# Optimization experiments

Hardware: AMD Instinct MI355X
Metric: run time of the kernel (lower is better)

The kernel has to match this reference:

```python
import jax, jax.numpy as jnp
import numpy as np

B, N, T, F = 4, 256, 16, 128
H = 256

def setup_inputs() -> dict:
    key = jax.random.key(0)
    k1, k2, k3, k4, k5 = jax.random.split(key, 5)
    bound1 = 1.0 / np.sqrt(2 * F)
    bound2 = 1.0 / np.sqrt(H)
    return {
        "nodefeat": jax.random.normal(k1, (B, N, T, F), dtype=jnp.float32),
        "W1": jax.random.uniform(k2, (H, 2 * F), minval=-bound1, maxval=bound1, dtype=jnp.float32),
        "b1": jax.random.uniform(k3, (H,), minval=-bound1, maxval=bound1, dtype=jnp.float32),
        "W2": jax.random.uniform(k4, (1, H), minval=-bound2, maxval=bound2, dtype=jnp.float32),
        "b2": jax.random.uniform(k5, (1,), minval=-bound2, maxval=bound2, dtype=jnp.float32),
    }

def reference(nodefeat, W1, b1, W2, b2):
    # nodefeat: [B,N,T,F] -> mean over time -> h: [B,N,F]
    h = jnp.mean(nodefeat, axis=2)
    f = h.shape[-1]
    # Split W1 to avoid materializing the [B,N,N,2F] concat:
    # Linear(cat(h_i,h_j)) = h_i @ W1[:, :F].T + h_j @ W1[:, F:].T + b1
    a = jnp.einsum('bnf,hf->bnh', h, W1[:, :f])  # contribution of h_i
    c = jnp.einsum('bnf,hf->bnh', h, W1[:, f:])  # contribution of h_j
    pre = a[:, :, None, :] + c[:, None, :, :] + b1  # [B,N,N,H]
    act = jax.nn.relu(pre)
    logits = jnp.einsum('bijh,h->bij', act, W2[0]) + b2[0]  # [B,N,N]
    return logits
```

## Files before the change

kernel.cpp:

```cpp
#include <hip/hip_runtime.h>

#define B_ 4
#define N_ 256
#define T_ 16
#define F_ 128
#define H_ 256
#define BN_ (B_ * N_)

__global__ __launch_bounds__(1024) void lp_prep(const float* __restrict__ nf,
                                                const float* __restrict__ W1,
                                                float* __restrict__ hbar,
                                                float* __restrict__ W1T) {
    __shared__ float sT[64][65];
    const int tid = threadIdx.x;
    if (blockIdx.x < 128) {
        const int idx = blockIdx.x * 1024 + tid;
        const int bn  = idx >> 7;
        const int f   = idx & 127;
        const float* src = nf + (size_t)bn * (T_ * F_) + f;
        float s = 0.f;
#pragma unroll
        for (int t = 0; t < T_; ++t) s += src[t * F_];
        hbar[idx] = s * (1.0f / 16.0f);
    } else {
        const int t  = blockIdx.x - 128;
        const int y0 = (t >> 2) * 64;
        const int x0 = (t & 3) * 64;
        const int ty = tid >> 6;
        const int tx = tid & 63;
#pragma unroll
        for (int r = 0; r < 4; ++r)
            sT[r * 16 + ty][tx] = W1[(size_t)(y0 + r * 16 + ty) * 256 + (x0 + tx)];
        __syncthreads();
#pragma unroll
        for (int r = 0; r < 4; ++r)
            W1T[(size_t)(x0 + r * 16 + ty) * 256 + (y0 + tx)] = sT[tx][r * 16 + ty];
    }
}

__global__ __launch_bounds__(512) void lp_gemm(const float* __restrict__ hbar,
                                               const float* __restrict__ W1T,
                                               const float* __restrict__ b1,
                                               float* __restrict__ aT,
                                               float* __restrict__ cT) {
    __shared__ float red[16][4][128];

    const int tile8 = blockIdx.x >> 1;
    const int h0    = (blockIdx.x & 1) * 128;
    const int bn0   = tile8 * 8;
    const int b     = bn0 >> 8;
    const int tid   = threadIdx.x;
    const int kq    = __builtin_amdgcn_readfirstlane(tid >> 7);
    const int hl    = tid & 127;
    const int h     = h0 + hl;

    const float* wA = W1T + (size_t)(kq * 32) * H_ + h;
    const float* wC = W1T + (size_t)(F_ + kq * 32) * H_ + h;
    const float* hb = hbar + (size_t)bn0 * F_ + kq * 32;

    float acca[8] = {0.f, 0.f, 0.f, 0.f, 0.f, 0.f, 0.f, 0.f};
    float accc[8] = {0.f, 0.f, 0.f, 0.f, 0.f, 0.f, 0.f, 0.f};

#pragma unroll 4
    for (int kk = 0; kk < 32; ++kk) {
        const float wa = wA[(size_t)kk * H_];
        const float wc = wC[(size_t)kk * H_];
#pragma unroll
        for (int n = 0; n < 8; ++n) {
            const float hv = hb[n * F_ + kk];
            acca[n] = fmaf(hv, wa, acca[n]);
            accc[n] = fmaf(hv, wc, accc[n]);
        }
    }

#pragma unroll
    for (int n = 0; n < 8; ++n) {
        red[n][kq][hl]     = acca[n];
        red[8 + n][kq][hl] = accc[n];
    }
    __syncthreads();

    const int rv = tid >> 7;
#pragma unroll
    for (int i = 0; i < 4; ++i) {
        const int v = rv * 4 + i;
        const float s = (red[v][0][hl] + red[v][1][hl]) + (red[v][2][hl] + red[v][3][hl]);
        if (v < 8) {
            const int bn = bn0 + v;
            aT[((size_t)(bn >> 2) * H_ + h) * 4 + (bn & 3)] = s + b1[h];
        } else {
            const int n = v - 8;
            cT[((size_t)b * H_ + h) * N_ + ((bn0 & 255) + n)] = s;
        }
    }
}

__global__ __launch_bounds__(1024) void lp_k2(const float* __restrict__ aT,
                                              const float* __restrict__ cT,
                                              const float* __restrict__ W2,
                                              const float* __restrict__ b2,
                                              float* __restrict__ out) {
    __shared__ float pr[8][8][128];

    const int bx  = blockIdx.x;
    const int b   = bx >> 6;
    const int rr  = bx & 63;
    const int it  = rr >> 1;
    const int jh  = rr & 1;
    const int i0  = it * 8;
    const int j0  = jh * 128;
    const int bn0 = b * N_ + i0;

    const int tid = threadIdx.x;
    const int ho  = __builtin_amdgcn_readfirstlane(tid >> 7);
    const int jl  = tid & 127;

    const float* crow = cT + (size_t)b * (H_ * N_) + j0 + jl;
    const float* a0 = aT + (size_t)(bn0 >> 2) * (H_ * 4);
    const float* a1 = a0 + H_ * 4;
    const int h0 = ho * 32;

    float acc0 = 0.f, acc1 = 0.f, acc2 = 0.f, acc3 = 0.f;
    float acc4 = 0.f, acc5 = 0.f, acc6 = 0.f, acc7 = 0.f;

#pragma unroll 4
    for (int hh = 0; hh < 32; ++hh) {
        const int h = h0 + hh;
        const float  cj  = crow[(size_t)h * N_];
        const float  w   = W2[h];
        const float4 av0 = *(const float4*)(a0 + h * 4);
        const float4 av1 = *(const float4*)(a1 + h * 4);
        float x;
        x = av0.x + cj; acc0 = fmaf(fmaxf(x, 0.f), w, acc0);
        x = av0.y + cj; acc1 = fmaf(fmaxf(x, 0.f), w, acc1);
        x = av0.z + cj; acc2 = fmaf(fmaxf(x, 0.f), w, acc2);
        x = av0.w + cj; acc3 = fmaf(fmaxf(x, 0.f), w, acc3);
        x = av1.x + cj; acc4 = fmaf(fmaxf(x, 0.f), w, acc4);
        x = av1.y + cj; acc5 = fmaf(fmaxf(x, 0.f), w, acc5);
        x = av1.z + cj; acc6 = fmaf(fmaxf(x, 0.f), w, acc6);
        x = av1.w + cj; acc7 = fmaf(fmaxf(x, 0.f), w, acc7);
    }

    pr[ho][0][jl] = acc0;
    pr[ho][1][jl] = acc1;
    pr[ho][2][jl] = acc2;
    pr[ho][3][jl] = acc3;
    pr[ho][4][jl] = acc4;
    pr[ho][5][jl] = acc5;
    pr[ho][6][jl] = acc6;
    pr[ho][7][jl] = acc7;
    __syncthreads();

    const int oi = tid >> 7;
    const int oj = tid & 127;
    float s = 0.f;
#pragma unroll
    for (int o = 0; o < 8; ++o) s += pr[o][oi][oj];
    out[(size_t)(bn0 + oi) * N_ + j0 + oj] = s + b2[0];
}

extern "C" void kernel_launch(void* const* d_in, const int* in_sizes, int n_in,
                              void* d_out, int out_size, void* d_ws, size_t ws_size,
                              hipStream_t stream) {
    const float* nodefeat = (const float*)d_in[0];
    const float* W1       = (const float*)d_in[1];
    const float* b1       = (const float*)d_in[2];
    const float* W2       = (const float*)d_in[3];
    const float* b2       = (const float*)d_in[4];
    float* out = (float*)d_out;

    float* hbar = (float*)d_ws;
    float* W1T  = hbar + (size_t)BN_ * F_;
    float* aT   = W1T + 256 * 256;
    float* cT   = aT + (size_t)256 * H_ * 4;

    lp_prep<<<144, 1024, 0, stream>>>(nodefeat, W1, hbar, W1T);
    lp_gemm<<<256, 512, 0, stream>>>(hbar, W1T, b1, aT, cT);
    lp_k2<<<256, 1024, 0, stream>>>(aT, cT, W2, b2, out);
}
```

Measured before the change: 25.45 us.

## Fuse time-mean, W1 transpose and projection GEMM into one kernel

Merges the prep kernel (time-mean plus W1 transpose) and the projection GEMM into a single kernel. Each block computes the time-mean for its 8 nodes into shared memory, then stages W1 in transposed 64-column chunks through LDS and accumulates the a/c projections, so the hbar and W1T round trips to global memory and one launch go away. In exchange, every one of the 128 blocks reloads and transposes all of W1, grid size drops from 256 to 128 blocks, and the large LDS buffer may limit occupancy.

```diff
diff --git a/kernel.cpp b/kernel.cpp
--- a/kernel.cpp
+++ b/kernel.cpp
@@ -5,92 +5,95 @@
 #define T_ 16
 #define F_ 128
 #define H_ 256
-#define BN_ (B_ * N_)
 
-__global__ __launch_bounds__(1024) void lp_prep(const float* __restrict__ nf,
-                                                const float* __restrict__ W1,
-                                                float* __restrict__ hbar,
-                                                float* __restrict__ W1T) {
-    __shared__ float sT[64][65];
+__global__ __launch_bounds__(1024) void lp_ka(const float* __restrict__ nf,
+                                              const float* __restrict__ W1,
+                                              const float* __restrict__ b1,
+                                              float* __restrict__ aT,
+                                              float* __restrict__ cT) {
+    __shared__ float sh[8 * 128];
+    __shared__ float buf[64 * 257];
+
+    const int blk = blockIdx.x;
+    const int bn0 = blk * 8;
+    const int b   = bn0 >> 8;
+    const int n0  = bn0 & 255;
     const int tid = threadIdx.x;
-    if (blockIdx.x < 128) {
-        const int idx = blockIdx.x * 1024 + tid;
-        const int bn  = idx >> 7;
-        const int f   = idx & 127;
-        const float* src = nf + (size_t)bn * (T_ * F_) + f;
+
+    {
+        const int n = tid >> 7;
+        const int f = tid & 127;
+        const float* src = nf + (size_t)(bn0 + n) * (T_ * F_) + f;
         float s = 0.f;
 #pragma unroll
         for (int t = 0; t < T_; ++t) s += src[t * F_];
-        hbar[idx] = s * (1.0f / 16.0f);
-    } else {
-        const int t  = blockIdx.x - 128;
-        const int y0 = (t >> 2) * 64;
-        const int x0 = (t & 3) * 64;
-        const int ty = tid >> 6;
-        const int tx = tid & 63;
-#pragma unroll
-        for (int r = 0; r < 4; ++r)
-            sT[r * 16 + ty][tx] = W1[(size_t)(y0 + r * 16 + ty) * 256 + (x0 + tx)];
-        __syncthreads();
-#pragma unroll
-        for (int r = 0; r < 4; ++r)
-            W1T[(size_t)(x0 + r * 16 + ty) * 256 + (y0 + tx)] = sT[tx][r * 16 + ty];
+        sh[n * 128 + f] = s * (1.0f / 16.0f);
     }
-}
 
-__global__ __launch_bounds__(512) void lp_gemm(const float* __restrict__ hbar,
-                                               const float* __restrict__ W1T,
-                                               const float* __restrict__ b1,
-                                               float* __restrict__ aT,
-                                               float* __restrict__ cT) {
-    __shared__ float red[16][4][128];
-
-    const int tile8 = blockIdx.x >> 1;
-    const int h0    = (blockIdx.x & 1) * 128;
-    const int bn0   = tile8 * 8;
-    const int b     = bn0 >> 8;
-    const int tid   = threadIdx.x;
-    const int kq    = __builtin_amdgcn_readfirstlane(tid >> 7);
-    const int hl    = tid & 127;
-    const int h     = h0 + hl;
-
-    const float* wA = W1T + (size_t)(kq * 32) * H_ + h;
-    const float* wC = W1T + (size_t)(F_ + kq * 32) * H_ + h;
-    const float* hb = hbar + (size_t)bn0 * F_ + kq * 32;
+    const int kq = tid >> 8;
+    const int h  = tid & 255;
 
     float acca[8] = {0.f, 0.f, 0.f, 0.f, 0.f, 0.f, 0.f, 0.f};
     float accc[8] = {0.f, 0.f, 0.f, 0.f, 0.f, 0.f, 0.f, 0.f};
 
-#pragma unroll 4
-    for (int kk = 0; kk < 32; ++kk) {
-        const float wa = wA[(size_t)kk * H_];
-        const float wc = wC[(size_t)kk * H_];
 #pragma unroll
-        for (int n = 0; n < 8; ++n) {
-            const float hv = hb[n * F_ + kk];
-            acca[n] = fmaf(hv, wa, acca[n]);
-            accc[n] = fmaf(hv, wc, accc[n]);
+    for (int c = 0; c < 4; ++c) {
+        __syncthreads();
+#pragma unroll
+        for (int i = 0; i < 4; ++i) {
+            const int e  = i * 1024 + tid;
+            const int hh = e >> 4;
+            const int f4 = e & 15;
+            const float4 w = *(const float4*)(W1 + (size_t)hh * 256 + c * 64 + f4 * 4);
+            const int k0 = f4 * 4;
+            buf[(k0 + 0) * 257 + hh] = w.x;
+            buf[(k0 + 1) * 257 + hh] = w.y;
+            buf[(k0 + 2) * 257 + hh] = w.z;
+            buf[(k0 + 3) * 257 + hh] = w.w;
+        }
+        __syncthreads();
+        const int kb = (c & 1) * 64 + kq * 16;
+        if (c < 2) {
+#pragma unroll
+            for (int kk = 0; kk < 16; ++kk) {
+                const float w = buf[(kq * 16 + kk) * 257 + h];
+                const int kh = kb + kk;
+#pragma unroll
+                for (int n = 0; n < 8; ++n)
+                    acca[n] = fmaf(sh[n * 128 + kh], w, acca[n]);
+            }
+        } else {
+#pragma unroll
+            for (int kk = 0; kk < 16; ++kk) {
+                const float w = buf[(kq * 16 + kk) * 257 + h];
+                const int kh = kb + kk;
+#pragma unroll
+                for (int n = 0; n < 8; ++n)
+                    accc[n] = fmaf(sh[n * 128 + kh], w, accc[n]);
+            }
         }
     }
 
+    __syncthreads();
 #pragma unroll
     for (int n = 0; n < 8; ++n) {
-        red[n][kq][hl]     = acca[n];
-        red[8 + n][kq][hl] = accc[n];
+        buf[((n)     * 4 + kq) * 256 + h] = acca[n];
+        buf[((8 + n) * 4 + kq) * 256 + h] = accc[n];
     }
     __syncthreads();
 
-    const int rv = tid >> 7;
 #pragma unroll
     for (int i = 0; i < 4; ++i) {
-        const int v = rv * 4 + i;
-        const float s = (red[v][0][hl] + red[v][1][hl]) + (red[v][2][hl] + red[v][3][hl]);
+        const int o  = i * 1024 + tid;
+        const int v  = o >> 8;
+        const int hh = o & 255;
+        const float* p = buf + v * 4 * 256 + hh;
+        const float s = (p[0] + p[256]) + (p[512] + p[768]);
         if (v < 8) {
             const int bn = bn0 + v;
-            aT[((size_t)(bn >> 2) * H_ + h) * 4 + (bn & 3)] = s + b1[h];
+            aT[((size_t)(bn >> 2) * H_ + hh) * 4 + (bn & 3)] = s + b1[hh];
         } else {
-            const int n = v - 8;
-            cT[((size_t)b * H_ + h) * N_ + ((bn0 & 255) + n)] = s;
+            cT[((size_t)b * H_ + hh) * N_ + (n0 + (v - 8))] = s;
         }
     }
 }
@@ -169,12 +172,9 @@
     const float* b2       = (const float*)d_in[4];
     float* out = (float*)d_out;
 
-    float* hbar = (float*)d_ws;
-    float* W1T  = hbar + (size_t)BN_ * F_;
-    float* aT   = W1T + 256 * 256;
-    float* cT   = aT + (size_t)256 * H_ * 4;
+    float* aT = (float*)d_ws;
+    float* cT = aT + (size_t)256 * H_ * 4;
 
-    lp_prep<<<144, 1024, 0, stream>>>(nodefeat, W1, hbar, W1T);
-    lp_gemm<<<256, 512, 0, stream>>>(hbar, W1T, b1, aT, cT);
+    lp_ka<<<128, 1024, 0, stream>>>(nodefeat, W1, b1, aT, cT);
     lp_k2<<<256, 1024, 0, stream>>>(aT, cT, W2, b2, out);
 }
```

Measured after the change: 26.72 us. +5.0%, slower.

## Rewrite relu as (x+|x|)/2 to factor linear terms; retile k2 and interleave cT

Applied to the files above, without the earlier changes.

The pairwise kernel now uses relu(x)=0.5*(x+|x|), so the linear part sum_h (a+c)*w2 splits into a per-row term (computed once per block with a wave reduction) and a per-column term accumulated alongside. The inner loop then needs only abs and fma. The c matrix is stored with pairs of h interleaved so each thread loads float2. k2 tiles change from 8 rows to 4 rows per block with twice as many blocks, raising parallelism at the cost of reloading c more often.

```diff
diff --git a/kernel.cpp b/kernel.cpp
--- a/kernel.cpp
+++ b/kernel.cpp
@@ -42,7 +42,7 @@
                                                const float* __restrict__ W1T,
                                                const float* __restrict__ b1,
                                                float* __restrict__ aT,
-                                               float* __restrict__ cT) {
+                                               float* __restrict__ cT2) {
     __shared__ float red[16][4][128];
 
     const int tile8 = blockIdx.x >> 1;
@@ -90,73 +90,92 @@
             aT[((size_t)(bn >> 2) * H_ + h) * 4 + (bn & 3)] = s + b1[h];
         } else {
             const int n = v - 8;
-            cT[((size_t)b * H_ + h) * N_ + ((bn0 & 255) + n)] = s;
+            cT2[(((size_t)b * (H_ / 2) + (h >> 1)) * N_ + ((bn0 & 255) + n)) * 2 + (h & 1)] = s;
         }
     }
 }
 
-__global__ __launch_bounds__(1024) void lp_k2(const float* __restrict__ aT,
-                                              const float* __restrict__ cT,
-                                              const float* __restrict__ W2,
-                                              const float* __restrict__ b2,
-                                              float* __restrict__ out) {
-    __shared__ float pr[8][8][128];
+__global__ __launch_bounds__(1024, 8) void lp_k2(const float* __restrict__ aT,
+                                                 const float* __restrict__ cT2,
+                                                 const float* __restrict__ W2,
+                                                 const float* __restrict__ b2,
+                                                 float* __restrict__ out) {
+    __shared__ float pr[8][5][128];
+    __shared__ float swu[16];
 
-    const int bx  = blockIdx.x;
-    const int b   = bx >> 6;
-    const int rr  = bx & 63;
-    const int it  = rr >> 1;
-    const int jh  = rr & 1;
-    const int i0  = it * 8;
-    const int j0  = jh * 128;
-    const int bn0 = b * N_ + i0;
+    const int bx    = blockIdx.x;
+    const int b     = bx >> 7;
+    const int rr    = bx & 127;
+    const int it    = rr >> 1;
+    const int jh    = rr & 1;
+    const int i0    = it * 4;
+    const int j0    = jh * 128;
+    const int bn0   = b * N_ + i0;
+    const int tile4 = bn0 >> 2;
 
     const int tid = threadIdx.x;
-    const int ho  = __builtin_amdgcn_readfirstlane(tid >> 7);
+    const float* atile = aT + (size_t)tile4 * (H_ * 4);
+
+    {
+        const int i  = tid >> 8;
+        const int hs = tid & 255;
+        float pa = atile[hs * 4 + i] * W2[hs];
+#pragma unroll
+        for (int off = 32; off >= 1; off >>= 1)
+            pa += __shfl_xor(pa, off, 64);
+        if ((tid & 63) == 0) swu[tid >> 6] = pa;
+    }
+
+    const int ho  = tid >> 7;
     const int jl  = tid & 127;
+    const int hp0 = ho * 16;
 
-    const float* crow = cT + (size_t)b * (H_ * N_) + j0 + jl;
-    const float* a0 = aT + (size_t)(bn0 >> 2) * (H_ * 4);
-    const float* a1 = a0 + H_ * 4;
-    const int h0 = ho * 32;
+    const float* cb   = cT2 + (((size_t)b * (H_ / 2) + hp0) * N_ + (j0 + jl)) * 2;
+    const float* arow = atile + hp0 * 8;
+    const float* w2p  = W2 + hp0 * 2;
 
-    float acc0 = 0.f, acc1 = 0.f, acc2 = 0.f, acc3 = 0.f;
-    float acc4 = 0.f, acc5 = 0.f, acc6 = 0.f, acc7 = 0.f;
+    float acc0 = 0.f, acc1 = 0.f, acc2 = 0.f, acc3 = 0.f, vacc = 0.f;
 
 #pragma unroll 4
-    for (int hh = 0; hh < 32; ++hh) {
-        const int h = h0 + hh;
-        const float  cj  = crow[(size_t)h * N_];
-        const float  w   = W2[h];
-        const float4 av0 = *(const float4*)(a0 + h * 4);
-        const float4 av1 = *(const float4*)(a1 + h * 4);
+    for (int p = 0; p < 16; ++p) {
+        const float2 cc = *(const float2*)(cb + (size_t)p * (N_ * 2));
+        const float4 aa = *(const float4*)(arow + p * 8);
+        const float4 ab = *(const float4*)(arow + p * 8 + 4);
+        const float  w0 = w2p[p * 2];
+        const float  w1 = w2p[p * 2 + 1];
         float x;
-        x = av0.x + cj; acc0 = fmaf(fmaxf(x, 0.f), w, acc0);
-        x = av0.y + cj; acc1 = fmaf(fmaxf(x, 0.f), w, acc1);
-        x = av0.z + cj; acc2 = fmaf(fmaxf(x, 0.f), w, acc2);
-        x = av0.w + cj; acc3 = fmaf(fmaxf(x, 0.f), w, acc3);
-        x = av1.x + cj; acc4 = fmaf(fmaxf(x, 0.f), w, acc4);
-        x = av1.y + cj; acc5 = fmaf(fmaxf(x, 0.f), w, acc5);
-        x = av1.z + cj; acc6 = fmaf(fmaxf(x, 0.f), w, acc6);
-        x = av1.w + cj; acc7 = fmaf(fmaxf(x, 0.f), w, acc7);
+        x = aa.x + cc.x; acc0 = fmaf(__builtin_fabsf(x), w0, acc0);
+        x = aa.y + cc.x; acc1 = fmaf(__builtin_fabsf(x), w0, acc1);
+        x = aa.z + cc.x; acc2 = fmaf(__builtin_fabsf(x), w0, acc2);
+        x = aa.w + cc.x; acc3 = fmaf(__builtin_fabsf(x), w0, acc3);
+        x = ab.x + cc.y; acc0 = fmaf(__builtin_fabsf(x), w1, acc0);
+        x = ab.y + cc.y; acc1 = fmaf(__builtin_fabsf(x), w1, acc1);
+        x = ab.z + cc.y; acc2 = fmaf(__builtin_fabsf(x), w1, acc2);
+        x = ab.w + cc.y; acc3 = fmaf(__builtin_fabsf(x), w1, acc3);
+        vacc = fmaf(cc.x, w0, vacc);
+        vacc = fmaf(cc.y, w1, vacc);
     }
 
     pr[ho][0][jl] = acc0;
     pr[ho][1][jl] = acc1;
     pr[ho][2][jl] = acc2;
     pr[ho][3][jl] = acc3;
-    pr[ho][4][jl] = acc4;
-    pr[ho][5][jl] = acc5;
-    pr[ho][6][jl] = acc6;
-    pr[ho][7][jl] = acc7;
+    pr[ho][4][jl] = vacc;
     __syncthreads();
 
-    const int oi = tid >> 7;
-    const int oj = tid & 127;
-    float s = 0.f;
+    if (tid < 512) {
+        const int oi = tid >> 7;
+        const int oj = tid & 127;
+        float s = 0.f, v = 0.f;
 #pragma unroll
-    for (int o = 0; o < 8; ++o) s += pr[o][oi][oj];
-    out[(size_t)(bn0 + oi) * N_ + j0 + oj] = s + b2[0];
+        for (int o = 0; o < 8; ++o) {
+            s += pr[o][oi][oj];
+            v += pr[o][4][oj];
+        }
+        const float u = (swu[oi * 4 + 0] + swu[oi * 4 + 1]) +
+                        (swu[oi * 4 + 2] + swu[oi * 4 + 3]);
+        out[(size_t)(bn0 + oi) * N_ + (j0 + oj)] = 0.5f * (s + v + u) + b2[0];
+    }
 }
 
 extern "C" void kernel_launch(void* const* d_in, const int* in_sizes, int n_in,
@@ -172,9 +191,9 @@
     float* hbar = (float*)d_ws;
     float* W1T  = hbar + (size_t)BN_ * F_;
     float* aT   = W1T + 256 * 256;
-    float* cT   = aT + (size_t)256 * H_ * 4;
+    float* cT2  = aT + (size_t)256 * H_ * 4;
 
     lp_prep<<<144, 1024, 0, stream>>>(nodefeat, W1, hbar, W1T);
-    lp_gemm<<<256, 512, 0, stream>>>(hbar, W1T, b1, aT, cT);
-    lp_k2<<<256, 1024, 0, stream>>>(aT, cT, W2, b2, out);
+    lp_gemm<<<256, 512, 0, stream>>>(hbar, W1T, b1, aT, cT2);
+    lp_k2<<<512, 1024, 0, stream>>>(aT, cT2, W2, b2, out);
 }
```

After: 32.80 us. 28.9% more time.
